# Kernel tuning notes

Measured on AMD Instinct MI355X. Metric: run time of the kernel, lower is better.

Reference implementation:

```python
import jax, jax.numpy as jnp
import numpy as np
from jax import lax

D_MODEL, D_STATE, D_CONV, EXPAND = 1024, 16, 4, 2
D_INNER = D_MODEL * EXPAND
B, L = 2, 1024


def setup_inputs() -> dict:
    key = jax.random.key(0)
    ks = jax.random.split(key, 8)
    x = jax.random.normal(ks[0], (B, L, D_MODEL), dtype=jnp.float32)
    # Linear weights stored as (in, out) so forward is x @ W
    in_proj_w = jax.random.normal(ks[1], (D_MODEL, 2 * D_INNER), jnp.float32) * (D_MODEL ** -0.5)
    conv_w = jax.random.normal(ks[2], (D_INNER, 1, D_CONV), jnp.float32) * (D_CONV ** -0.5)  # depthwise, OIH
    conv_b = jax.random.normal(ks[3], (D_INNER,), jnp.float32) * 0.02
    x_proj_w = jax.random.normal(ks[4], (D_INNER, 1 + 2 * D_STATE), jnp.float32) * (D_INNER ** -0.5)
    dt_w = jax.random.normal(ks[5], (D_INNER,), jnp.float32)  # Linear(1, d_inner) weight
    dt_b = jax.random.normal(ks[6], (D_INNER,), jnp.float32) * 0.02
    A = jnp.arange(1, D_STATE + 1, dtype=jnp.float32)[None, :] * jnp.ones((D_INNER, 1), jnp.float32)
    A_log = jnp.clip(jnp.log(A), -6.0, 6.0)
    Dp = jnp.ones((D_INNER,), jnp.float32)
    out_proj_w = jax.random.normal(ks[7], (D_INNER, D_MODEL), jnp.float32) * (D_INNER ** -0.5)
    return dict(x=x, in_proj_w=in_proj_w, conv_w=conv_w, conv_b=conv_b,
                x_proj_w=x_proj_w, dt_w=dt_w, dt_b=dt_b, A_log=A_log, D=Dp,
                out_proj_w=out_proj_w)


def reference(x, in_proj_w, conv_w, conv_b, x_proj_w, dt_w, dt_b, A_log, D, out_proj_w):
    x = x.astype(jnp.float32)
    b, l, _ = x.shape
    S = D_STATE
    xz = x @ in_proj_w                      # [B, L, 2*d_inner]
    xi, z = jnp.split(xz, 2, axis=-1)
    # causal depthwise conv1d: left-pad d_conv-1, output length L
    xc = lax.conv_general_dilated(
        jnp.transpose(xi, (0, 2, 1)), conv_w,
        window_strides=(1,), padding=[(D_CONV - 1, 0)],
        dimension_numbers=('NCH', 'OIH', 'NCH'),
        feature_group_count=D_INNER)
    xc = jnp.transpose(xc + conv_b[None, :, None], (0, 2, 1))  # [B, L, d_inner]
    xc = jax.nn.silu(xc)
    bcdt = xc @ x_proj_w                     # [B, L, 1+2S]
    dt_raw, Bs, Cs = bcdt[..., :1], bcdt[..., 1:1 + S], bcdt[..., 1 + S:]
    dt = jax.nn.softplus(dt_raw * dt_w + dt_b)   # [B, L, d_inner]
    A = -jnp.exp(jnp.clip(A_log, -6.0, 6.0))     # [d_inner, S]
    dA = jnp.exp(dt[..., None] * A[None, None])              # [B, L, d_inner, S]
    dBx = dt[..., None] * Bs[:, :, None, :] * xc[..., None]  # [B, L, d_inner, S]

    def step(h, inp):
        dA_t, dBx_t, C_t = inp              # [B,d,S], [B,d,S], [B,S]
        h = jnp.clip(dA_t * h + dBx_t, -10000.0, 10000.0)
        y = jnp.einsum('bds,bs->bd', h, C_t)
        return h, y

    h0 = jnp.zeros((b, D_INNER, S), jnp.float32)
    xs = (jnp.moveaxis(dA, 1, 0), jnp.moveaxis(dBx, 1, 0), jnp.moveaxis(Cs, 1, 0))
    _, ys = lax.scan(step, h0, xs)           # [L, B, d_inner]
    y = jnp.moveaxis(ys, 0, 1) + xc * D[None, None]
    y = y * jax.nn.silu(z)
    return y @ out_proj_w
```

## Files before the change

### kernel.cpp

```cpp
#include <hip/hip_runtime.h>
#include <hip/hip_bf16.h>
#include <math.h>

#define D_MODEL 1024
#define D_STATE 16
#define D_CONV 4
#define D_INNER 2048
#define BATCH 2
#define LEN 1024
#define ROWS (BATCH * LEN)
#define N_XZ (2 * D_INNER)
#define N_BCDT (1 + 2 * D_STATE)
#define BSTRIDE 48
#define KSPLIT 8
#define KSEG (D_INNER / KSPLIT)
#define NCHUNK 32
#define CHUNK (LEN / NCHUNK)

using bf16x8 = __attribute__((ext_vector_type(8))) short;
using f32x4  = __attribute__((ext_vector_type(4))) float;
using u16x4  = __attribute__((ext_vector_type(4))) unsigned short;

__device__ __forceinline__ float sigmoidf_(float x) {
    return 1.0f / (1.0f + __expf(-x));
}

__device__ __forceinline__ unsigned short f2bf(float f) {
    unsigned u = __float_as_uint(f);
    unsigned r = (u + 0x7FFFu + ((u >> 16) & 1u)) >> 16;
    return (unsigned short)r;
}

__global__ __launch_bounds__(256) void prep(const float* __restrict__ x,
                                            const float* __restrict__ w1,
                                            const float* __restrict__ w2,
                                            const float* __restrict__ xpw,
                                            unsigned short* __restrict__ xbf,
                                            unsigned short* __restrict__ w1t,
                                            unsigned short* __restrict__ w2t,
                                            unsigned short* __restrict__ wbc) {
    __shared__ float tile[32][33];
    const int blk = blockIdx.x;
    const int tid = threadIdx.x;
    if (blk < 1024) {
        int i = (blk * 256 + tid) * 8;
        float4 f0 = *(const float4*)&x[i];
        float4 f1 = *(const float4*)&x[i + 4];
        bf16x8 v;
        v[0] = (short)f2bf(f0.x); v[1] = (short)f2bf(f0.y);
        v[2] = (short)f2bf(f0.z); v[3] = (short)f2bf(f0.w);
        v[4] = (short)f2bf(f1.x); v[5] = (short)f2bf(f1.y);
        v[6] = (short)f2bf(f1.z); v[7] = (short)f2bf(f1.w);
        *(bf16x8*)&xbf[i] = v;
    } else if (blk < 5120) {
        int t = blk - 1024;
        int c0 = (t & 127) * 32, r0 = (t >> 7) * 32;
        int tx = tid & 31, ty = tid >> 5;
        #pragma unroll
        for (int k = 0; k < 32; k += 8)
            tile[ty + k][tx] = w1[(size_t)(r0 + ty + k) * N_XZ + c0 + tx];
        __syncthreads();
        #pragma unroll
        for (int k = 0; k < 32; k += 8)
            w1t[(size_t)(c0 + ty + k) * D_MODEL + r0 + tx] = f2bf(tile[tx][ty + k]);
    } else if (blk < 7168) {
        int t = blk - 5120;
        int c0 = (t & 31) * 32, r0 = (t >> 5) * 32;
        int tx = tid & 31, ty = tid >> 5;
        #pragma unroll
        for (int k = 0; k < 32; k += 8)
            tile[ty + k][tx] = w2[(size_t)(r0 + ty + k) * D_MODEL + c0 + tx];
        __syncthreads();
        #pragma unroll
        for (int k = 0; k < 32; k += 8)
            w2t[(size_t)(c0 + ty + k) * D_INNER + r0 + tx] = f2bf(tile[tx][ty + k]);
    } else {
        int j = blk - 7168;
        if (j < N_BCDT) {
            for (int k = tid; k < D_INNER; k += 256)
                wbc[(size_t)j * D_INNER + k] = f2bf(xpw[(size_t)k * N_BCDT + j]);
        } else {
            for (int k = tid; k < D_INNER; k += 256)
                wbc[(size_t)j * D_INNER + k] = 0;
        }
    }
}

template<int BM, int BN, int WM, int WN>
__global__ __launch_bounds__(256) void gemm_bf16_t(const unsigned short* __restrict__ A,
                                                   const unsigned short* __restrict__ BT,
                                                   float* __restrict__ C,
                                                   int M, int N, int K) {
    constexpr int FM = WM / 16;
    constexpr int FN = WN / 16;
    constexpr int NWC = BN / WN;
    __shared__ __align__(16) short sA[BM][64];
    __shared__ __align__(16) short sB[BN][64];
    const int tid = threadIdx.x;
    const int bm = blockIdx.y * BM;
    const int bn = blockIdx.x * BN;
    const int lane = tid & 63;
    const int w = tid >> 6;
    const int wrow = (w / NWC) * WM;
    const int wcol = (w % NWC) * WN;
    const int laneRow = lane & 15;
    const int half8 = (lane >> 4) * 8;
    const int swzR = (laneRow & 7) << 3;

    f32x4 acc[FM][FN] = {};

    for (int k0 = 0; k0 < K; k0 += 64) {
        #pragma unroll
        for (int i = 0; i < BM / 32; i++) {
            int q = tid + i * 256;
            int sr = q >> 3, sc = (q & 7) * 8;
            int gc = sc ^ ((sr & 7) << 3);
            __builtin_amdgcn_global_load_lds(
                (const __attribute__((address_space(1))) void*)(A + (size_t)(bm + sr) * K + k0 + gc),
                (__attribute__((address_space(3))) void*)&sA[sr][sc], 16, 0, 0);
        }
        #pragma unroll
        for (int i = 0; i < BN / 32; i++) {
            int q = tid + i * 256;
            int sr = q >> 3, sc = (q & 7) * 8;
            int gc = sc ^ ((sr & 7) << 3);
            __builtin_amdgcn_global_load_lds(
                (const __attribute__((address_space(1))) void*)(BT + (size_t)(bn + sr) * K + k0 + gc),
                (__attribute__((address_space(3))) void*)&sB[sr][sc], 16, 0, 0);
        }
        __syncthreads();

        #pragma unroll
        for (int kblk = 0; kblk < 2; kblk++) {
            const int cbase = (kblk * 32 + half8) ^ swzR;
            bf16x8 af[FM], bfr[FN];
            #pragma unroll
            for (int i = 0; i < FM; i++)
                af[i] = *(const bf16x8*)&sA[wrow + i * 16 + laneRow][cbase];
            #pragma unroll
            for (int j = 0; j < FN; j++)
                bfr[j] = *(const bf16x8*)&sB[wcol + j * 16 + laneRow][cbase];
            #pragma unroll
            for (int i = 0; i < FM; i++)
                #pragma unroll
                for (int j = 0; j < FN; j++)
                    acc[i][j] = __builtin_amdgcn_mfma_f32_16x16x32_bf16(af[i], bfr[j], acc[i][j], 0, 0, 0);
        }
        __syncthreads();
    }

    const int crow0 = bm + wrow + (lane >> 4) * 4;
    const int ccol0 = bn + wcol + laneRow;
    #pragma unroll
    for (int i = 0; i < FM; i++)
        #pragma unroll
        for (int j = 0; j < FN; j++)
            #pragma unroll
            for (int q = 0; q < 4; q++)
                C[(size_t)(crow0 + i * 16 + q) * N + ccol0 + j * 16] = acc[i][j][q];
}

__global__ __launch_bounds__(256) void conv_silu(const float* __restrict__ xz,
                                                 const float* __restrict__ conv_w,
                                                 const float* __restrict__ conv_b,
                                                 float* __restrict__ xc,
                                                 unsigned short* __restrict__ xcb) {
    int gid = blockIdx.x * 256 + threadIdx.x;
    int d4 = (gid & 511) * 4;
    int row = gid >> 9;
    int l = row & (LEN - 1);

    float4 acc = *(const float4*)&conv_b[d4];
    #pragma unroll
    for (int j = 0; j < D_CONV; j++) {
        int lp = l - (D_CONV - 1) + j;
        if (lp >= 0) {
            float4 xv = *(const float4*)&xz[(size_t)(row - (D_CONV - 1) + j) * N_XZ + d4];
            acc.x = fmaf(xv.x, conv_w[(d4 + 0) * D_CONV + j], acc.x);
            acc.y = fmaf(xv.y, conv_w[(d4 + 1) * D_CONV + j], acc.y);
            acc.z = fmaf(xv.z, conv_w[(d4 + 2) * D_CONV + j], acc.z);
            acc.w = fmaf(xv.w, conv_w[(d4 + 3) * D_CONV + j], acc.w);
        }
    }
    acc.x *= sigmoidf_(acc.x);
    acc.y *= sigmoidf_(acc.y);
    acc.z *= sigmoidf_(acc.z);
    acc.w *= sigmoidf_(acc.w);
    *(float4*)&xc[(size_t)row * D_INNER + d4] = acc;
    u16x4 bv = {f2bf(acc.x), f2bf(acc.y), f2bf(acc.z), f2bf(acc.w)};
    *(u16x4*)&xcb[(size_t)row * D_INNER + d4] = bv;
}

__global__ __launch_bounds__(256) void bcdt_gemm(const unsigned short* __restrict__ xcb,
                                                 const unsigned short* __restrict__ wbc,
                                                 float* __restrict__ part) {
    __shared__ __align__(16) short sA[64][64];
    __shared__ __align__(16) short sB[48][64];
    const int tid = threadIdx.x;
    const int kseg = blockIdx.x;
    const int bm = blockIdx.y * 64;
    const int lane = tid & 63;
    const int w = tid >> 6;
    const int laneRow = lane & 15;
    const int half8 = (lane >> 4) * 8;
    const int swzR = (laneRow & 7) << 3;

    f32x4 acc[3] = {};

    for (int k0 = kseg * KSEG; k0 < kseg * KSEG + KSEG; k0 += 64) {
        {
            #pragma unroll
            for (int i = 0; i < 2; i++) {
                int q = tid + i * 256;
                int sr = q >> 3, sc = (q & 7) * 8;
                int gc = sc ^ ((sr & 7) << 3);
                __builtin_amdgcn_global_load_lds(
                    (const __attribute__((address_space(1))) void*)(xcb + (size_t)(bm + sr) * D_INNER + k0 + gc),
                    (__attribute__((address_space(3))) void*)&sA[sr][sc], 16, 0, 0);
            }
        }
        {
            int q = tid;
            int sr = q >> 3, sc = (q & 7) * 8;
            int gc = sc ^ ((sr & 7) << 3);
            __builtin_amdgcn_global_load_lds(
                (const __attribute__((address_space(1))) void*)(wbc + (size_t)sr * D_INNER + k0 + gc),
                (__attribute__((address_space(3))) void*)&sB[sr][sc], 16, 0, 0);
            q = tid + 256;
            if (q < 384) {
                sr = q >> 3; sc = (q & 7) * 8;
                gc = sc ^ ((sr & 7) << 3);
                __builtin_amdgcn_global_load_lds(
                    (const __attribute__((address_space(1))) void*)(wbc + (size_t)sr * D_INNER + k0 + gc),
                    (__attribute__((address_space(3))) void*)&sB[sr][sc], 16, 0, 0);
            }
        }
        __syncthreads();

        #pragma unroll
        for (int kblk = 0; kblk < 2; kblk++) {
            const int cbase = (kblk * 32 + half8) ^ swzR;
            bf16x8 af = *(const bf16x8*)&sA[w * 16 + laneRow][cbase];
            #pragma unroll
            for (int j = 0; j < 3; j++) {
                bf16x8 bfr = *(const bf16x8*)&sB[j * 16 + laneRow][cbase];
                acc[j] = __builtin_amdgcn_mfma_f32_16x16x32_bf16(af, bfr, acc[j], 0, 0, 0);
            }
        }
        __syncthreads();
    }

    const int crow0 = bm + w * 16 + (lane >> 4) * 4;
    #pragma unroll
    for (int j = 0; j < 3; j++)
        #pragma unroll
        for (int q = 0; q < 4; q++)
            part[((size_t)kseg * ROWS + crow0 + q) * BSTRIDE + j * 16 + laneRow] = acc[j][q];
}

__global__ __launch_bounds__(256) void bcdt_reduce(const float* __restrict__ part,
                                                   float* __restrict__ bcdt) {
    int i = blockIdx.x * 256 + threadIdx.x;
    float s = 0.f;
    #pragma unroll
    for (int g = 0; g < KSPLIT; g++) s += part[(size_t)g * ROWS * BSTRIDE + i];
    bcdt[i] = s;
}

__global__ __launch_bounds__(256) void scan_stageA(const float* __restrict__ bcdt,
                                                   const float* __restrict__ xc,
                                                   const float* __restrict__ dt_w,
                                                   const float* __restrict__ dt_b,
                                                   float* __restrict__ aArr,
                                                   float* __restrict__ hpArr) {
    const int cg = blockIdx.x * 256 + threadIdx.x;
    const int b = blockIdx.y;
    const int g = blockIdx.z;
    const float dtw = dt_w[cg], dtb = dt_b[cg];
    const int t0 = g * CHUNK;

    float hp[16];
    #pragma unroll
    for (int s = 0; s < 16; s++) hp[s] = 0.f;
    float dtSum = 0.f;

    const float* __restrict__ rowp = bcdt + (size_t)(b * LEN + t0) * BSTRIDE;
    const float* __restrict__ xcp  = xc + (size_t)(b * LEN + t0) * D_INNER + cg;

    for (int t = 0; t < CHUNK; t++) {
        float dtr = rowp[0];
        float u = fmaf(dtr, dtw, dtb);
        float dt = (u > 20.f) ? u : __logf(1.f + __expf(u));
        float e1 = __expf(-dt);
        float xvv = xcp[0];
        float dtx = dt * xvv;
        dtSum += dt;
        float e = e1;
        #pragma unroll
        for (int s = 0; s < 16; s++) {
            hp[s] = fmaf(e, hp[s], dtx * rowp[1 + s]);
            e *= e1;
        }
        rowp += BSTRIDE;
        xcp += D_INNER;
    }

    float E = __expf(-dtSum);
    float a_[16];
    float e = E;
    #pragma unroll
    for (int s = 0; s < 16; s++) { a_[s] = e; e *= E; }

    size_t o = (((size_t)(b * NCHUNK + g) * D_INNER) + cg) * 16;
    #pragma unroll
    for (int q = 0; q < 4; q++) {
        *(f32x4*)&aArr[o + q * 4]  = *(f32x4*)&a_[q * 4];
        *(f32x4*)&hpArr[o + q * 4] = *(f32x4*)&hp[q * 4];
    }
}

__global__ __launch_bounds__(256) void scan_chain(const float* __restrict__ aArr,
                                                  const float* __restrict__ hpArr,
                                                  float* __restrict__ hIn) {
    int idx = blockIdx.x * 256 + threadIdx.x;
    int b = idx >> 15;
    int rem = idx & 32767;
    float h = 0.f;
    #pragma unroll 4
    for (int g = 0; g < NCHUNK; g++) {
        size_t o = ((size_t)(b * NCHUNK + g) << 15) + rem;
        hIn[o] = h;
        h = fmaf(aArr[o], h, hpArr[o]);
    }
}

__global__ __launch_bounds__(256) void scan_stageC(const float* __restrict__ bcdt,
                                                   const float* __restrict__ xc,
                                                   const float* __restrict__ xz,
                                                   const float* __restrict__ dt_w,
                                                   const float* __restrict__ dt_b,
                                                   const float* __restrict__ Dp,
                                                   const float* __restrict__ hIn,
                                                   unsigned short* __restrict__ ybf) {
    const int cg = blockIdx.x * 256 + threadIdx.x;
    const int b = blockIdx.y;
    const int g = blockIdx.z;
    const float dtw = dt_w[cg], dtb = dt_b[cg], Dv = Dp[cg];
    const int t0 = g * CHUNK;

    float h[16];
    size_t o = (((size_t)(b * NCHUNK + g) * D_INNER) + cg) * 16;
    #pragma unroll
    for (int q = 0; q < 4; q++)
        *(f32x4*)&h[q * 4] = *(const f32x4*)&hIn[o + q * 4];

    const float* __restrict__ rowp = bcdt + (size_t)(b * LEN + t0) * BSTRIDE;
    const float* __restrict__ xcp  = xc + (size_t)(b * LEN + t0) * D_INNER + cg;
    const float* __restrict__ zp   = xz + (size_t)(b * LEN + t0) * N_XZ + D_INNER + cg;
    unsigned short* __restrict__ yp = ybf + (size_t)(b * LEN + t0) * D_INNER + cg;

    for (int t = 0; t < CHUNK; t++) {
        float dtr = rowp[0];
        float u = fmaf(dtr, dtw, dtb);
        float dt = (u > 20.f) ? u : __logf(1.f + __expf(u));
        float e1 = __expf(-dt);
        float xvv = xcp[0];
        float dtx = dt * xvv;
        float y = 0.f;
        float e = e1;
        #pragma unroll
        for (int s = 0; s < 16; s++) {
            h[s] = fminf(fmaxf(fmaf(e, h[s], dtx * rowp[1 + s]), -10000.f), 10000.f);
            y = fmaf(h[s], rowp[17 + s], y);
            e *= e1;
        }
        float zv = zp[0];
        float gt = zv * sigmoidf_(zv);
        float yo = (y + xvv * Dv) * gt;
        yp[0] = f2bf(yo);
        rowp += BSTRIDE;
        xcp += D_INNER;
        zp += N_XZ;
        yp += D_INNER;
    }
}

extern "C" void kernel_launch(void* const* d_in, const int* in_sizes, int n_in,
                              void* d_out, int out_size, void* d_ws, size_t ws_size,
                              hipStream_t stream) {
    const float* x         = (const float*)d_in[0];
    const float* in_proj_w = (const float*)d_in[1];
    const float* conv_w    = (const float*)d_in[2];
    const float* conv_b    = (const float*)d_in[3];
    const float* x_proj_w  = (const float*)d_in[4];
    const float* dt_w      = (const float*)d_in[5];
    const float* dt_b      = (const float*)d_in[6];
    const float* A_log     = (const float*)d_in[7];
    const float* Dp        = (const float*)d_in[8];
    const float* out_proj_w= (const float*)d_in[9];
    float* out = (float*)d_out;
    (void)A_log;

    float* ws = (float*)d_ws;
    float* xz    = ws;
    float* xc    = xz + (size_t)ROWS * N_XZ;
    float* bcdt  = xc + (size_t)ROWS * D_INNER;
    float* aArr  = bcdt + (size_t)ROWS * BSTRIDE;
    float* hpArr = aArr + (size_t)BATCH * NCHUNK * D_INNER * 16;
    float* hIn   = hpArr + (size_t)BATCH * NCHUNK * D_INNER * 16;
    unsigned short* w1t = (unsigned short*)(hIn + (size_t)BATCH * NCHUNK * D_INNER * 16);
    unsigned short* w2t = w1t + (size_t)N_XZ * D_MODEL;
    unsigned short* xbf = w2t + (size_t)D_MODEL * D_INNER;
    unsigned short* ybf = xbf + (size_t)ROWS * D_MODEL;
    unsigned short* wbc = ybf + (size_t)ROWS * D_INNER;
    float* part = aArr;
    unsigned short* xcb = (unsigned short*)hpArr;

    prep<<<7216, 256, 0, stream>>>(x, in_proj_w, out_proj_w, x_proj_w, xbf, w1t, w2t, wbc);

    gemm_bf16_t<128, 128, 64, 64><<<dim3(N_XZ / 128, ROWS / 128), 256, 0, stream>>>(
        xbf, w1t, xz, ROWS, N_XZ, D_MODEL);

    conv_silu<<<(ROWS * (D_INNER / 4)) / 256, 256, 0, stream>>>(xz, conv_w, conv_b, xc, xcb);

    bcdt_gemm<<<dim3(KSPLIT, ROWS / 64), 256, 0, stream>>>(xcb, wbc, part);
    bcdt_reduce<<<(ROWS * BSTRIDE) / 256, 256, 0, stream>>>(part, bcdt);

    scan_stageA<<<dim3(D_INNER / 256, BATCH, NCHUNK), 256, 0, stream>>>(bcdt, xc, dt_w, dt_b, aArr, hpArr);
    scan_chain<<<(BATCH * D_INNER * 16) / 256, 256, 0, stream>>>(aArr, hpArr, hIn);
    scan_stageC<<<dim3(D_INNER / 256, BATCH, NCHUNK), 256, 0, stream>>>(bcdt, xc, xz, dt_w, dt_b, Dp, hIn, ybf);

    gemm_bf16_t<64, 128, 32, 64><<<dim3(D_MODEL / 128, ROWS / 64), 256, 0, stream>>>(
        ybf, w2t, out, ROWS, D_MODEL, D_INNER);
}
```

Baseline: 245.0 us.

## Vectorize weight transpose, register-block conv, drop fp32 xc, enlarge in_proj tile

The weight-transpose prep now uses 64x64 tiles with float4 loads and 8-wide bf16 stores instead of scalar 32x32 tiles. conv_silu computes four rows per thread, reusing seven loaded taps and vectorized conv weights. It writes only the bf16 xc, and both scan stages read that bf16 copy instead of a separate fp32 buffer, cutting memory traffic. The in_proj GEMM switches to a 256x128 block tile, and the scan now uses bf16-rounded xc, which may slightly shift numerical accuracy.

```diff
diff --git a/kernel.cpp b/kernel.cpp
--- a/kernel.cpp
+++ b/kernel.cpp
@@ -20,6 +20,7 @@
 using bf16x8 = __attribute__((ext_vector_type(8))) short;
 using f32x4  = __attribute__((ext_vector_type(4))) float;
 using u16x4  = __attribute__((ext_vector_type(4))) unsigned short;
+using u16x8  = __attribute__((ext_vector_type(8))) unsigned short;
 
 __device__ __forceinline__ float sigmoidf_(float x) {
     return 1.0f / (1.0f + __expf(-x));
@@ -29,6 +30,9 @@
     unsigned u = __float_as_uint(f);
     unsigned r = (u + 0x7FFFu + ((u >> 16) & 1u)) >> 16;
     return (unsigned short)r;
+}
+__device__ __forceinline__ float bf2f(unsigned short v) {
+    return __uint_as_float(((unsigned)v) << 16);
 }
 
 __global__ __launch_bounds__(256) void prep(const float* __restrict__ x,
@@ -39,7 +43,7 @@
                                             unsigned short* __restrict__ w1t,
                                             unsigned short* __restrict__ w2t,
                                             unsigned short* __restrict__ wbc) {
-    __shared__ float tile[32][33];
+    __shared__ float tile[64][65];
     const int blk = blockIdx.x;
     const int tid = threadIdx.x;
     if (blk < 1024) {
@@ -52,30 +56,10 @@
         v[4] = (short)f2bf(f1.x); v[5] = (short)f2bf(f1.y);
         v[6] = (short)f2bf(f1.z); v[7] = (short)f2bf(f1.w);
         *(bf16x8*)&xbf[i] = v;
-    } else if (blk < 5120) {
-        int t = blk - 1024;
-        int c0 = (t & 127) * 32, r0 = (t >> 7) * 32;
-        int tx = tid & 31, ty = tid >> 5;
-        #pragma unroll
-        for (int k = 0; k < 32; k += 8)
-            tile[ty + k][tx] = w1[(size_t)(r0 + ty + k) * N_XZ + c0 + tx];
-        __syncthreads();
-        #pragma unroll
-        for (int k = 0; k < 32; k += 8)
-            w1t[(size_t)(c0 + ty + k) * D_MODEL + r0 + tx] = f2bf(tile[tx][ty + k]);
-    } else if (blk < 7168) {
-        int t = blk - 5120;
-        int c0 = (t & 31) * 32, r0 = (t >> 5) * 32;
-        int tx = tid & 31, ty = tid >> 5;
-        #pragma unroll
-        for (int k = 0; k < 32; k += 8)
-            tile[ty + k][tx] = w2[(size_t)(r0 + ty + k) * D_MODEL + c0 + tx];
-        __syncthreads();
-        #pragma unroll
-        for (int k = 0; k < 32; k += 8)
-            w2t[(size_t)(c0 + ty + k) * D_INNER + r0 + tx] = f2bf(tile[tx][ty + k]);
-    } else {
-        int j = blk - 7168;
+        return;
+    }
+    if (blk >= 2560) {
+        int j = blk - 2560;
         if (j < N_BCDT) {
             for (int k = tid; k < D_INNER; k += 256)
                 wbc[(size_t)j * D_INNER + k] = f2bf(xpw[(size_t)k * N_BCDT + j]);
@@ -83,6 +67,40 @@
             for (int k = tid; k < D_INNER; k += 256)
                 wbc[(size_t)j * D_INNER + k] = 0;
         }
+        return;
+    }
+    const float* src; unsigned short* dst; int R, C, r0, c0;
+    if (blk < 2048) {
+        int t = blk - 1024;
+        src = w1; dst = w1t; R = 1024; C = 4096;
+        r0 = (t >> 6) * 64; c0 = (t & 63) * 64;
+    } else {
+        int t = blk - 2048;
+        src = w2; dst = w2t; R = 2048; C = 1024;
+        r0 = (t >> 4) * 64; c0 = (t & 15) * 64;
+    }
+    {
+        int r = tid >> 2, cs = (tid & 3) * 16;
+        #pragma unroll
+        for (int q = 0; q < 4; q++) {
+            float4 v = *(const float4*)&src[(size_t)(r0 + r) * C + c0 + cs + q * 4];
+            tile[r][cs + q * 4 + 0] = v.x;
+            tile[r][cs + q * 4 + 1] = v.y;
+            tile[r][cs + q * 4 + 2] = v.z;
+            tile[r][cs + q * 4 + 3] = v.w;
+        }
+    }
+    __syncthreads();
+    {
+        int c = tid >> 2, rs = (tid & 3) * 16;
+        u16x8 o0, o1;
+        #pragma unroll
+        for (int i = 0; i < 8; i++) {
+            o0[i] = f2bf(tile[rs + i][c]);
+            o1[i] = f2bf(tile[rs + 8 + i][c]);
+        }
+        *(u16x8*)&dst[(size_t)(c0 + c) * R + r0 + rs] = o0;
+        *(u16x8*)&dst[(size_t)(c0 + c) * R + r0 + rs + 8] = o1;
     }
 }
 
@@ -163,32 +181,44 @@
 __global__ __launch_bounds__(256) void conv_silu(const float* __restrict__ xz,
                                                  const float* __restrict__ conv_w,
                                                  const float* __restrict__ conv_b,
-                                                 float* __restrict__ xc,
                                                  unsigned short* __restrict__ xcb) {
     int gid = blockIdx.x * 256 + threadIdx.x;
     int d4 = (gid & 511) * 4;
-    int row = gid >> 9;
-    int l = row & (LEN - 1);
-
-    float4 acc = *(const float4*)&conv_b[d4];
-    #pragma unroll
-    for (int j = 0; j < D_CONV; j++) {
-        int lp = l - (D_CONV - 1) + j;
-        if (lp >= 0) {
-            float4 xv = *(const float4*)&xz[(size_t)(row - (D_CONV - 1) + j) * N_XZ + d4];
-            acc.x = fmaf(xv.x, conv_w[(d4 + 0) * D_CONV + j], acc.x);
-            acc.y = fmaf(xv.y, conv_w[(d4 + 1) * D_CONV + j], acc.y);
-            acc.z = fmaf(xv.z, conv_w[(d4 + 2) * D_CONV + j], acc.z);
-            acc.w = fmaf(xv.w, conv_w[(d4 + 3) * D_CONV + j], acc.w);
-        }
-    }
-    acc.x *= sigmoidf_(acc.x);
-    acc.y *= sigmoidf_(acc.y);
-    acc.z *= sigmoidf_(acc.z);
-    acc.w *= sigmoidf_(acc.w);
-    *(float4*)&xc[(size_t)row * D_INNER + d4] = acc;
-    u16x4 bv = {f2bf(acc.x), f2bf(acc.y), f2bf(acc.z), f2bf(acc.w)};
-    *(u16x4*)&xcb[(size_t)row * D_INNER + d4] = bv;
+    int r0 = (gid >> 9) * 4;
+    int l0 = r0 & (LEN - 1);
+
+    float4 taps[7];
+    #pragma unroll
+    for (int i = 0; i < 7; i++) {
+        int l = l0 - 3 + i;
+        if (l >= 0)
+            taps[i] = *(const float4*)&xz[(size_t)(r0 - 3 + i) * N_XZ + d4];
+        else
+            taps[i] = float4{0.f, 0.f, 0.f, 0.f};
+    }
+    float4 bb = *(const float4*)&conv_b[d4];
+    float4 wc[4];
+    #pragma unroll
+    for (int c = 0; c < 4; c++) wc[c] = *(const float4*)&conv_w[(d4 + c) * 4];
+
+    #pragma unroll
+    for (int ro = 0; ro < 4; ro++) {
+        float a0 = bb.x, a1 = bb.y, a2 = bb.z, a3 = bb.w;
+        #pragma unroll
+        for (int j = 0; j < 4; j++) {
+            float4 tp = taps[ro + j];
+            a0 = fmaf(tp.x, ((const float*)&wc[0])[j], a0);
+            a1 = fmaf(tp.y, ((const float*)&wc[1])[j], a1);
+            a2 = fmaf(tp.z, ((const float*)&wc[2])[j], a2);
+            a3 = fmaf(tp.w, ((const float*)&wc[3])[j], a3);
+        }
+        a0 *= sigmoidf_(a0);
+        a1 *= sigmoidf_(a1);
+        a2 *= sigmoidf_(a2);
+        a3 *= sigmoidf_(a3);
+        u16x4 bv = {f2bf(a0), f2bf(a1), f2bf(a2), f2bf(a3)};
+        *(u16x4*)&xcb[(size_t)(r0 + ro) * D_INNER + d4] = bv;
+    }
 }
 
 __global__ __launch_bounds__(256) void bcdt_gemm(const unsigned short* __restrict__ xcb,
@@ -268,7 +298,7 @@
 }
 
 __global__ __launch_bounds__(256) void scan_stageA(const float* __restrict__ bcdt,
-                                                   const float* __restrict__ xc,
+                                                   const unsigned short* __restrict__ xcb,
                                                    const float* __restrict__ dt_w,
                                                    const float* __restrict__ dt_b,
                                                    float* __restrict__ aArr,
@@ -285,14 +315,14 @@
     float dtSum = 0.f;
 
     const float* __restrict__ rowp = bcdt + (size_t)(b * LEN + t0) * BSTRIDE;
-    const float* __restrict__ xcp  = xc + (size_t)(b * LEN + t0) * D_INNER + cg;
+    const unsigned short* __restrict__ xcp = xcb + (size_t)(b * LEN + t0) * D_INNER + cg;
 
     for (int t = 0; t < CHUNK; t++) {
         float dtr = rowp[0];
         float u = fmaf(dtr, dtw, dtb);
         float dt = (u > 20.f) ? u : __logf(1.f + __expf(u));
         float e1 = __expf(-dt);
-        float xvv = xcp[0];
+        float xvv = bf2f(xcp[0]);
         float dtx = dt * xvv;
         dtSum += dt;
         float e = e1;
@@ -335,7 +365,7 @@
 }
 
 __global__ __launch_bounds__(256) void scan_stageC(const float* __restrict__ bcdt,
-                                                   const float* __restrict__ xc,
+                                                   const unsigned short* __restrict__ xcb,
                                                    const float* __restrict__ xz,
                                                    const float* __restrict__ dt_w,
                                                    const float* __restrict__ dt_b,
@@ -355,7 +385,7 @@
         *(f32x4*)&h[q * 4] = *(const f32x4*)&hIn[o + q * 4];
 
     const float* __restrict__ rowp = bcdt + (size_t)(b * LEN + t0) * BSTRIDE;
-    const float* __restrict__ xcp  = xc + (size_t)(b * LEN + t0) * D_INNER + cg;
+    const unsigned short* __restrict__ xcp = xcb + (size_t)(b * LEN + t0) * D_INNER + cg;
     const float* __restrict__ zp   = xz + (size_t)(b * LEN + t0) * N_XZ + D_INNER + cg;
     unsigned short* __restrict__ yp = ybf + (size_t)(b * LEN + t0) * D_INNER + cg;
 
@@ -364,7 +394,7 @@
         float u = fmaf(dtr, dtw, dtb);
         float dt = (u > 20.f) ? u : __logf(1.f + __expf(u));
         float e1 = __expf(-dt);
-        float xvv = xcp[0];
+        float xvv = bf2f(xcp[0]);
         float dtx = dt * xvv;
         float y = 0.f;
         float e = e1;
@@ -403,8 +433,7 @@
 
     float* ws = (float*)d_ws;
     float* xz    = ws;
-    float* xc    = xz + (size_t)ROWS * N_XZ;
-    float* bcdt  = xc + (size_t)ROWS * D_INNER;
+    float* bcdt  = xz + (size_t)ROWS * N_XZ;
     float* aArr  = bcdt + (size_t)ROWS * BSTRIDE;
     float* hpArr = aArr + (size_t)BATCH * NCHUNK * D_INNER * 16;
     float* hIn   = hpArr + (size_t)BATCH * NCHUNK * D_INNER * 16;
@@ -413,22 +442,22 @@
     unsigned short* xbf = w2t + (size_t)D_MODEL * D_INNER;
     unsigned short* ybf = xbf + (size_t)ROWS * D_MODEL;
     unsigned short* wbc = ybf + (size_t)ROWS * D_INNER;
+    unsigned short* xcb = wbc + (size_t)48 * D_INNER;
     float* part = aArr;
-    unsigned short* xcb = (unsigned short*)hpArr;
-
-    prep<<<7216, 256, 0, stream>>>(x, in_proj_w, out_proj_w, x_proj_w, xbf, w1t, w2t, wbc);
-
-    gemm_bf16_t<128, 128, 64, 64><<<dim3(N_XZ / 128, ROWS / 128), 256, 0, stream>>>(
+
+    prep<<<2608, 256, 0, stream>>>(x, in_proj_w, out_proj_w, x_proj_w, xbf, w1t, w2t, wbc);
+
+    gemm_bf16_t<256, 128, 64, 128><<<dim3(N_XZ / 128, ROWS / 256), 256, 0, stream>>>(
         xbf, w1t, xz, ROWS, N_XZ, D_MODEL);
 
-    conv_silu<<<(ROWS * (D_INNER / 4)) / 256, 256, 0, stream>>>(xz, conv_w, conv_b, xc, xcb);
+    conv_silu<<<(ROWS / 4) * (D_INNER / 4) / 256, 256, 0, stream>>>(xz, conv_w, conv_b, xcb);
 
     bcdt_gemm<<<dim3(KSPLIT, ROWS / 64), 256, 0, stream>>>(xcb, wbc, part);
     bcdt_reduce<<<(ROWS * BSTRIDE) / 256, 256, 0, stream>>>(part, bcdt);
 
-    scan_stageA<<<dim3(D_INNER / 256, BATCH, NCHUNK), 256, 0, stream>>>(bcdt, xc, dt_w, dt_b, aArr, hpArr);
+    scan_stageA<<<dim3(D_INNER / 256, BATCH, NCHUNK), 256, 0, stream>>>(bcdt, xcb, dt_w, dt_b, aArr, hpArr);
     scan_chain<<<(BATCH * D_INNER * 16) / 256, 256, 0, stream>>>(aArr, hpArr, hIn);
-    scan_stageC<<<dim3(D_INNER / 256, BATCH, NCHUNK), 256, 0, stream>>>(bcdt, xc, xz, dt_w, dt_b, Dp, hIn, ybf);
+    scan_stageC<<<dim3(D_INNER / 256, BATCH, NCHUNK), 256, 0, stream>>>(bcdt, xcb, xz, dt_w, dt_b, Dp, hIn, ybf);
 
     gemm_bf16_t<64, 128, 32, 64><<<dim3(D_MODEL / 128, ROWS / 64), 256, 0, stream>>>(
         ybf, w2t, out, ROWS, D_MODEL, D_INNER);
```

New measurement: 224.8 us. -8.2%, faster.
